# Kernel optimization log

Measured on AMD Instinct MI355X. Metric: run time of the kernel, lower is better.

The kernel has to match this reference:

```python
import jax, jax.numpy as jnp
import numpy as np

B, N, K = 4, 8192, 10
_DIMS = [(12, 64), (64, 64), (128, 64), (64, 64), (128, 64), (192, 1024), (1216, 256), (256, 256), (256, 128), (128, 2)]


def setup_inputs() -> dict:
    key = jax.random.key(0)
    keys = jax.random.split(key, 12)
    inp = {"targets": jax.random.normal(keys[0], (B, N, 3), dtype=jnp.float32)}
    for i, (ci, co) in enumerate(_DIMS):
        a = float(np.sqrt(0.75 / ci))  # init_params: uniform(-sqrt(0.75/fan_in), +)
        inp[f"w{i + 1}"] = jax.random.uniform(keys[i + 1], (ci, co), minval=-a, maxval=a, dtype=jnp.float32)
    inp["prelu_a"] = 0.25 * jnp.ones((10,), jnp.float32)  # nn.PReLU default slope
    return inp


def _prelu(x, a):
    return jnp.where(x >= 0, x, a * x)


def _graph_features(x, k):
    # x: [N, C] -> edge features [N, k, 2C] (knn gather, diff, concat center)
    x2 = jnp.sum(x * x, axis=-1)
    d = x2[:, None] + x2[None, :] - 2.0 * (x @ x.T)  # [N, N] sq dists
    _, idx = jax.lax.top_k(-d, k)  # k nearest (includes self)
    nb = x[idx]  # [N, k, C]
    xr = jnp.broadcast_to(x[:, None, :], nb.shape)
    return jnp.concatenate([nb - xr, xr], axis=-1)


def _edge_conv(x, wa_list, k):
    # x: [B, N, C]; shared-MLP on edge features then max over k neighbors
    f = jax.vmap(lambda xb: _graph_features(xb, k))(x)  # [B, N, k, 2C]
    for w, a in wa_list:
        f = _prelu(f @ w, a)
    return jnp.max(f, axis=-2)  # [B, N, Cout]


def _forward(targets, ws, pa):
    # loss_f(targets) = 0.5*||targets||^2  =>  targets_grad = targets
    g = jax.grad(lambda t: 0.5 * jnp.sum(t * t))(targets)
    x = jnp.concatenate([targets, g], axis=-1)  # [B, N, 6]; hidden_features=0
    x1 = _edge_conv(x, [(ws[0], pa[0]), (ws[1], pa[1])], K)
    x2 = _edge_conv(x1, [(ws[2], pa[2]), (ws[3], pa[3])], K)
    x3 = _edge_conv(x2, [(ws[4], pa[4])], K)
    x4 = jnp.concatenate([x1, x2, x3], axis=-1)  # [B, N, 192]
    x5 = _prelu(x4 @ ws[5], pa[5])  # [B, N, 1024]
    x5 = jnp.broadcast_to(jnp.max(x5, axis=-2, keepdims=True), x5.shape)  # global max, repeated
    y = jnp.concatenate([x1, x2, x3, x5], axis=-1)  # [B, N, 1216]
    for i in range(6, 10):  # dropout is identity at eval
        y = _prelu(y @ ws[i], pa[i])
    return y[..., : 2]  # lr = y[..., :num_losses*2]; hidden slice is empty


def reference(targets, w1, w2, w3, w4, w5, w6, w7, w8, w9, w10, prelu_a):
    ws = [w1, w2, w3, w4, w5, w6, w7, w8, w9, w10]
    return _forward(targets, ws, prelu_a)
```

## Files before the change

kernel.cpp:

```cpp
#include <hip/hip_runtime.h>
#include <math.h>

#define NPTS 8192
#define KNNK 10

typedef __attribute__((ext_vector_type(8))) short bf16x8s;
typedef __attribute__((ext_vector_type(4))) float f32x4;

__device__ __forceinline__ float preluf(float v, float a){ return v >= 0.f ? v : a*v; }
__device__ __forceinline__ float4 f4fma(float a, float4 b, float4 c){
  return make_float4(fmaf(a,b.x,c.x), fmaf(a,b.y,c.y), fmaf(a,b.z,c.z), fmaf(a,b.w,c.w));
}

__device__ __forceinline__ void gl_lds16(const void* g, void* l){
  __builtin_amdgcn_global_load_lds((const __attribute__((address_space(1))) void*)g,
                                   (__attribute__((address_space(3))) void*)l, 16, 0, 0);
}
__device__ __forceinline__ void gl_lds4(const void* g, void* l){
  __builtin_amdgcn_global_load_lds((const __attribute__((address_space(1))) void*)g,
                                   (__attribute__((address_space(3))) void*)l, 4, 0, 0);
}

__device__ __forceinline__ void kinsd2(double* bk, float& g9, float pbd9, float d, int j){
  if (__any(d < g9)) {
    double t = (double)d;
    t = __longlong_as_double(__double_as_longlong(t) | (unsigned long long)(unsigned)j);
    #pragma unroll
    for (int s=0;s<10;++s){
      double mn = fmin(bk[s], t);
      double mx = fmax(bk[s], t);
      bk[s] = mn; t = mx;
    }
    g9 = fminf((float)bk[9], pbd9);
  }
}

__device__ __forceinline__ unsigned bfsplit2(float a, float b, unsigned& lo2){
  unsigned ua = __float_as_uint(a), ub = __float_as_uint(b);
  unsigned ha = (ua + 0x7FFFu + ((ua>>16)&1u)) & 0xFFFF0000u;
  unsigned hb = (ub + 0x7FFFu + ((ub>>16)&1u)) & 0xFFFF0000u;
  float ra = a - __uint_as_float(ha);
  float rb = b - __uint_as_float(hb);
  unsigned la = __float_as_uint(ra), lb = __float_as_uint(rb);
  unsigned qa = (la + 0x7FFFu + ((la>>16)&1u)) >> 16;
  unsigned qb = (lb + 0x7FFFu + ((lb>>16)&1u)) & 0xFFFF0000u;
  lo2 = qa | qb;
  return (ha >> 16) | hb;
}

__global__ __launch_bounds__(256) void prep0_kernel(const float* __restrict__ T,
                                                    float* __restrict__ x0,
                                                    float* __restrict__ sqn){
  int p = blockIdx.x*256 + threadIdx.x;
  float t0 = T[p*3+0], t1 = T[p*3+1], t2 = T[p*3+2];
  *(float4*)(x0 + (size_t)p*4) = make_float4(t0,t1,t2,0.f);
  float s = fmaf(t0,t0,0.f); s = fmaf(t1,t1,s); s = fmaf(t2,t2,s); s = fmaf(0.f,0.f,s);
  sqn[p] = s;
}

__global__ __launch_bounds__(256, 4) void knn64_kernel(const unsigned short* __restrict__ Xh,
                                                       const unsigned short* __restrict__ Xl,
                                                       const float* __restrict__ sqn,
                                                       double* __restrict__ pk){
  __shared__ __align__(16) unsigned char smem[33792];
  float* sx2j = (float*)(smem + 32768);
  double* lst = (double*)smem;

  const int b   = blockIdx.y;
  const int q0  = blockIdx.x * 64;
  const int jh  = blockIdx.z;
  const int tid = threadIdx.x;
  const int L   = tid & 63;
  const int w   = tid >> 6;
  const int lm  = L & 15;
  const int kg  = L >> 4;

  const size_t bbase = (size_t)b * NPTS;
  const int qi = q0 + w*16 + lm;

  bf16x8s qh[2], ql[2];
  {
    const char* Qh = (const char*)Xh + (bbase + qi)*128;
    const char* Ql = (const char*)Xl + (bbase + qi)*128;
    #pragma unroll
    for (int kc=0;kc<2;++kc){
      qh[kc] = *(const bf16x8s*)(Qh + kc*64 + kg*16);
      ql[kc] = *(const bf16x8s*)(Ql + kc*64 + kg*16);
    }
  }
  const float x2q = sqn[bbase + qi];

  const int srow = L >> 3;
  const unsigned soff = (unsigned)(((L & 7) ^ srow) << 4);
  const char* srch = (const char*)Xh + (bbase + (size_t)jh*4096 + w*32 + srow)*128 + soff;
  const char* srcl = (const char*)Xl + (bbase + (size_t)jh*4096 + w*32 + srow)*128 + soff;
  const float* sx2jsrc = sqn + bbase + jh*4096 + w*64 + L;

  #pragma unroll
  for (int i=0;i<4;++i){
    gl_lds16(srch + i*1024, smem + w*4096 + i*1024);
    gl_lds16(srcl + i*1024, smem + 16384 + w*4096 + i*1024);
  }
  if (w < 2) gl_lds4(sx2jsrc, (char*)sx2j + w*256);

  double bk[10];
  float g9 = INFINITY, pbd9 = INFINITY;
  #pragma unroll
  for (int u=0;u<10;++u) bk[u] = (double)INFINITY;

  const char* xjh_c = (const char*)smem;
  const char* xjl_c = (const char*)smem + 16384;
  const unsigned swz = (unsigned)((lm & 7) << 4);

  for (int t = 0; t < 32; ++t) {
    __syncthreads();

    f32x4 acc[8];
    #pragma unroll
    for (int jb=0;jb<8;++jb) acc[jb] = (f32x4){0.f,0.f,0.f,0.f};

    #pragma unroll
    for (int kc=0;kc<2;++kc){
      const unsigned koff = (unsigned)(kc*64 + kg*16) ^ swz;
      #pragma unroll
      for (int jb=0;jb<8;++jb){
        const int rb = (jb*16 + lm)*128;
        bf16x8s jhf = *(const bf16x8s*)(xjh_c + rb + koff);
        bf16x8s jlf = *(const bf16x8s*)(xjl_c + rb + koff);
        acc[jb] = __builtin_amdgcn_mfma_f32_16x16x32_bf16(jhf, qh[kc], acc[jb], 0,0,0);
        acc[jb] = __builtin_amdgcn_mfma_f32_16x16x32_bf16(jlf, qh[kc], acc[jb], 0,0,0);
        acc[jb] = __builtin_amdgcn_mfma_f32_16x16x32_bf16(jhf, ql[kc], acc[jb], 0,0,0);
      }
    }
    __syncthreads();

    if (t < 31){
      const char* nh = srch + (size_t)(t+1)*16384;
      const char* nl = srcl + (size_t)(t+1)*16384;
      #pragma unroll
      for (int i=0;i<4;++i){
        gl_lds16(nh + i*1024, smem + w*4096 + i*1024);
        gl_lds16(nl + i*1024, smem + 16384 + w*4096 + i*1024);
      }
      if (w < 2) gl_lds4(sx2jsrc + (size_t)(t+1)*128, (char*)sx2j + ((t+1)&1)*512 + w*256);
    }

    const int j0 = jh*4096 + t*128;
    const float* x2jb = sx2j + (t&1)*128;

    #pragma unroll
    for (int jb=0;jb<8;++jb){
      float4 xj2 = *(const float4*)&x2jb[jb*16 + kg*4];
      f32x4 c = acc[jb];
      float4 dv = make_float4(x2q + xj2.x - 2.0f*c[0],
                              x2q + xj2.y - 2.0f*c[1],
                              x2q + xj2.z - 2.0f*c[2],
                              x2q + xj2.w - 2.0f*c[3]);
      float m4 = fminf(fminf(dv.x,dv.y), fminf(dv.z,dv.w));
      if (__any(m4 < g9)){
        const int jj = j0 + jb*16 + kg*4;
        kinsd2(bk, g9, pbd9, dv.x, jj);
        kinsd2(bk, g9, pbd9, dv.y, jj+1);
        kinsd2(bk, g9, pbd9, dv.z, jj+2);
        kinsd2(bk, g9, pbd9, dv.w, jj+3);
      }
      if (jb & 1){
        float d9 = (float)bk[9];
        float m  = fminf(d9, __shfl_xor(d9, 16));
        float mm = fminf(m,  __shfl_xor(m, 32));
        pbd9 = mm;
        g9 = mm;
      }
    }
  }

  __syncthreads();
  #pragma unroll
  for (int u=0;u<10;++u) lst[(size_t)(w*16 + lm)*40 + kg*10 + u] = bk[u];
  __syncthreads();
  if (tid < 64) {
    const double* row = &lst[(size_t)tid*40];
    int i0=0, i1=0, i2=0, i3=0;
    size_t base = ((size_t)jh*(4*NPTS) + bbase + q0 + tid)*10;
    #pragma unroll
    for (int u=0;u<10;++u){
      double ka = row[i0], kb2 = row[10+i1], kc2 = row[20+i2], kd2 = row[30+i3];
      bool tab = ka  < kb2; double mab = tab ? ka  : kb2;
      bool tcd = kc2 < kd2; double mcd = tcd ? kc2 : kd2;
      bool tt  = mab < mcd; double m   = tt  ? mab : mcd;
      pk[base+u] = m;
      i0 += (tt && tab)  ? 1 : 0;
      i1 += (tt && !tab) ? 1 : 0;
      i2 += (!tt && tcd) ? 1 : 0;
      i3 += (!tt && !tcd)? 1 : 0;
    }
  }
}

__global__ __launch_bounds__(256, 2) void knn4_kernel(const float* __restrict__ X,
                                                      const float* __restrict__ sqn,
                                                      double* __restrict__ pk){
  __shared__ __align__(16) float xqT[4*132];
  __shared__ __align__(16) float uni[10752];
  __shared__ float s_x2q[128];
  __shared__ float s_x2j[128];
  __shared__ float sbd[2][128];

  const int b   = blockIdx.y;
  const int q0  = blockIdx.x * 128;
  const int jh  = blockIdx.z;
  const int tid = threadIdx.x;
  const int tn  = tid & 15;
  const int tm  = tid >> 4;
  const int tq  = tid & 127;
  const int th  = tid >> 7;

  const float* Xb = X + (size_t)b * NPTS * 4;

  for (int i = tid; i < 128; i += 256) {
    float4 v = *(const float4*)(Xb + (size_t)(q0+i)*4);
    xqT[0*132+i] = v.x; xqT[1*132+i] = v.y; xqT[2*132+i] = v.z; xqT[3*132+i] = v.w;
  }
  if (tid < 128) s_x2q[tid] = sqn[b*NPTS + q0 + tid];

  const int sw  = ((tn>>2)&3) << 2;
  const int bp0 = (tn*8)     ^ sw;
  const int bp1 = (tn*8 + 4) ^ sw;

  double bk[10];
  float g9 = INFINITY, pbd9 = INFINITY;
  #pragma unroll
  for (int u=0;u<10;++u) bk[u] = (double)INFINITY;

  for (int t = 0; t < 32; ++t) {
    const int j0 = jh*4096 + t*128;
    for (int i = tid; i < 128; i += 256) {
      float4 v = *(const float4*)(Xb + (size_t)(j0+i)*4);
      int pj = i ^ (((i>>5)&3) << 2);
      uni[0*132+pj] = v.x; uni[1*132+pj] = v.y; uni[2*132+pj] = v.z; uni[3*132+pj] = v.w;
    }
    if (tid < 128) s_x2j[tid] = sqn[b*NPTS + j0 + tid];
    __syncthreads();

    float acc[8][8];
    #pragma unroll
    for (int i=0;i<8;++i)
      #pragma unroll
      for (int j=0;j<8;++j) acc[i][j] = 0.f;

    #pragma unroll
    for (int kk=0; kk<4; ++kk) {
      float av[8], bv[8];
      *(float4*)&av[0] = *(const float4*)&xqT[kk*132 + tm*8];
      *(float4*)&av[4] = *(const float4*)&xqT[kk*132 + tm*8 + 4];
      *(float4*)&bv[0] = *(const float4*)&uni[kk*132 + bp0];
      *(float4*)&bv[4] = *(const float4*)&uni[kk*132 + bp1];
      #pragma unroll
      for (int i=0;i<8;++i)
        #pragma unroll
        for (int j=0;j<8;++j)
          acc[i][j] = fmaf(av[i], bv[j], acc[i][j]);
    }
    __syncthreads();

    #pragma unroll
    for (int h=0; h<2; ++h) {
      if ((tn>>3) == h) {
        #pragma unroll
        for (int qi=0; qi<8; ++qi) {
          const int row = tm*8 + qi;
          const float xq2 = s_x2q[row];
          float vv[8];
          #pragma unroll
          for (int u=0;u<8;++u)
            vv[u] = xq2 + s_x2j[tn*8 + u] - 2.f*acc[qi][u];
          *(float4*)&uni[row*68 + (tn&7)*8]     = make_float4(vv[0],vv[1],vv[2],vv[3]);
          *(float4*)&uni[row*68 + (tn&7)*8 + 4] = make_float4(vv[4],vv[5],vv[6],vv[7]);
        }
      }
      __syncthreads();
      {
        const int jb0 = j0 + h*64 + th*32;
        #pragma unroll
        for (int c4=0;c4<8;++c4){
          float4 dv = *(const float4*)&uni[tq*68 + th*32 + c4*4];
          int jj = jb0 + c4*4;
          kinsd2(bk, g9, pbd9, dv.x, jj);
          kinsd2(bk, g9, pbd9, dv.y, jj+1);
          kinsd2(bk, g9, pbd9, dv.z, jj+2);
          kinsd2(bk, g9, pbd9, dv.w, jj+3);
        }
      }
      if (h == 1) sbd[th][tq] = (float)bk[9];
      __syncthreads();
      if (h == 1){
        pbd9 = sbd[1^th][tq];
        g9 = fminf((float)bk[9], pbd9);
      }
    }
  }

  double* lst = (double*)uni;
  #pragma unroll
  for (int u=0;u<10;++u) lst[tq*20 + th*10 + u] = bk[u];
  __syncthreads();
  if (tid < 128) {
    const double* row = &lst[tid*20];
    int ia=0, ib=0;
    size_t base = ((size_t)jh*(4*NPTS) + (size_t)b*NPTS + q0 + tid)*10;
    #pragma unroll
    for (int u=0;u<10;++u){
      double ka = row[ia], kb2 = row[10+ib];
      bool ta = ka < kb2;
      pk[base+u] = ta ? ka : kb2;
      ia += ta ? 1 : 0; ib += ta ? 0 : 1;
    }
  }
}

__global__ __launch_bounds__(256) void knnmerge_kernel(const double* __restrict__ pk,
                                                       int* __restrict__ idxout){
  int p = blockIdx.x*256 + threadIdx.x;
  const double* A = pk + (size_t)p*10;
  const double* B = pk + (size_t)(4*NPTS)*10 + (size_t)p*10;
  int ia=0, ib=0;
  int* op = idxout + (size_t)p*10;
  #pragma unroll
  for (int u=0;u<10;++u){
    double ka = A[ia], kb = B[ib];
    bool t = ka < kb;
    op[u] = (int)(__double_as_longlong(t ? ka : kb) & 8191LL);
    ia += t ? 1 : 0; ib += t ? 0 : 1;
  }
}

__global__ __launch_bounds__(256) void prepUD64_kernel(const float* __restrict__ XC, int cin,
                                                       const float* __restrict__ W,
                                                       float* __restrict__ U,
                                                       float* __restrict__ D){
  const int tid = threadIdx.x;
  const int w = tid >> 6, o = tid & 63;
  const int p = blockIdx.x*4 + w;
  const float* xr = XC + (size_t)p*192 + cin;
  float zu = 0.f, zd = 0.f;
  #pragma unroll
  for (int c=0;c<64;++c){
    float xc = xr[c];
    float wt = W[c*64 + o];
    float wb = W[(64+c)*64 + o];
    zu = fmaf(xc, wt, zu);
    zd = fmaf(xc, wb - wt, zd);
  }
  U[(size_t)p*64 + o] = zu;
  D[(size_t)p*64 + o] = zd;
}

__global__ __launch_bounds__(256) void prepUD12_kernel(const float* __restrict__ T,
                                                       const float* __restrict__ W1,
                                                       float* __restrict__ U,
                                                       float* __restrict__ D){
  int p = blockIdx.x*256 + threadIdx.x;
  float t[3] = {T[p*3+0], T[p*3+1], T[p*3+2]};
  const float4* W = (const float4*)W1;
  float4 u[16], q[16];
  #pragma unroll
  for (int o=0;o<16;++o){ u[o]=make_float4(0,0,0,0); q[o]=make_float4(0,0,0,0); }
  #pragma unroll
  for (int c=0;c<3;++c){
    const float tc = t[c];
    #pragma unroll
    for (int o=0;o<16;++o){
      float4 ws  = W[c*16+o],     ws2 = W[(c+3)*16+o];
      float4 wq  = W[(c+6)*16+o], wq2 = W[(c+9)*16+o];
      u[o] = f4fma(tc, make_float4(ws.x+ws2.x, ws.y+ws2.y, ws.z+ws2.z, ws.w+ws2.w), u[o]);
      q[o] = f4fma(tc, make_float4(wq.x+wq2.x, wq.y+wq2.y, wq.z+wq2.z, wq.w+wq2.w), q[o]);
    }
  }
  float4* up = (float4*)(U + (size_t)p*64);
  float4* dp = (float4*)(D + (size_t)p*64);
  #pragma unroll
  for (int o=0;o<16;++o){
    up[o] = u[o];
    dp[o] = make_float4(q[o].x-u[o].x, q[o].y-u[o].y, q[o].z-u[o].z, q[o].w-u[o].w);
  }
}

__global__ __launch_bounds__(256) void edge2w_kernel(const float* __restrict__ U,
                                                     const float* __restrict__ Dp,
                                                     const int* __restrict__ idx,
                                                     const float* __restrict__ Wb,
                                                     const float* __restrict__ PA, int paa, int pab,
                                                     float* __restrict__ out, int coff,
                                                     float* __restrict__ sqnout,
                                                     unsigned short* __restrict__ Xh,
                                                     unsigned short* __restrict__ Xl){
  __shared__ __align__(16) float sh[4][10][68];
  const int tid = threadIdx.x;
  const int w = tid >> 6, o = tid & 63;
  const int p = blockIdx.x*4 + w, b = p >> 13;
  const float aa = PA[paa], ab = PA[pab];

  float wreg[64];
  #pragma unroll
  for (int c=0;c<64;++c) wreg[c] = Wb[c*64 + o];

  const float dc = Dp[(size_t)p*64 + o];

  #pragma unroll
  for (int k=0;k<10;++k){
    int nb = idx[p*10 + k];
    float u = U[((size_t)(b<<13)+nb)*64 + o];
    sh[w][k][o] = preluf(u + dc, aa);
  }
  __syncthreads();

  float mx = -INFINITY;
  #pragma unroll 2
  for (int k=0;k<10;++k){
    float a0=0.f,a1=0.f,a2=0.f,a3=0.f;
    #pragma unroll
    for (int c4=0;c4<16;++c4){
      float4 hv = *(const float4*)&sh[w][k][c4*4];
      a0 = fmaf(hv.x, wreg[c4*4+0], a0);
      a1 = fmaf(hv.y, wreg[c4*4+1], a1);
      a2 = fmaf(hv.z, wreg[c4*4+2], a2);
      a3 = fmaf(hv.w, wreg[c4*4+3], a3);
    }
    float z = (a0+a1)+(a2+a3);
    mx = fmaxf(mx, preluf(z, ab));
  }
  out[(size_t)p*192 + coff + o] = mx;
  {
    unsigned um = __float_as_uint(mx);
    unsigned h  = (um + 0x7FFFu + ((um>>16)&1u)) & 0xFFFF0000u;
    float rr = mx - __uint_as_float(h);
    unsigned ur = __float_as_uint(rr);
    unsigned l  = (ur + 0x7FFFu + ((ur>>16)&1u)) >> 16;
    Xh[(size_t)p*64 + o] = (unsigned short)(h >> 16);
    Xl[(size_t)p*64 + o] = (unsigned short)l;
  }
  float sq = mx*mx;
  #pragma unroll
  for (int off=1; off<64; off<<=1) sq += __shfl_xor(sq, off);
  if (o == 0) sqnout[p] = sq;
}

__global__ __launch_bounds__(256) void edge1w_kernel(const float* __restrict__ U,
                                                     const float* __restrict__ Dp,
                                                     const int* __restrict__ idx,
                                                     const float* __restrict__ PA, int paa,
                                                     float* __restrict__ out, int coff){
  const int tid = threadIdx.x;
  const int w = tid >> 6, o = tid & 63;
  const int p = blockIdx.x*4 + w, b = p >> 13;
  const float aa = PA[paa];
  const float dc = Dp[(size_t)p*64 + o];
  float mx = -INFINITY;
  #pragma unroll
  for (int k=0;k<10;++k){
    int nb = idx[p*10 + k];
    float u = U[((size_t)(b<<13)+nb)*64 + o];
    mx = fmaxf(mx, preluf(u + dc, aa));
  }
  out[(size_t)p*192 + coff + o] = mx;
}

__global__ __launch_bounds__(256) void prepWall_kernel(const float* __restrict__ W6,
                                                       const float* __restrict__ W7,
                                                       const float* __restrict__ W8,
                                                       const float* __restrict__ W9,
                                                       unsigned short* __restrict__ Wh6, unsigned short* __restrict__ Wl6,
                                                       unsigned short* __restrict__ Wh7, unsigned short* __restrict__ Wl7,
                                                       unsigned short* __restrict__ Wh8, unsigned short* __restrict__ Wl8,
                                                       unsigned short* __restrict__ Wh9, unsigned short* __restrict__ Wl9){
  int bb = blockIdx.x;
  const float* W; unsigned short *Wh, *Wl; int K, N, k;
  if (bb < 192)      { W=W6; Wh=Wh6; Wl=Wl6; K=192; N=1024; k=bb; }
  else if (bb < 384) { W=W7; Wh=Wh7; Wl=Wl7; K=192; N=256;  k=bb-192; }
  else if (bb < 640) { W=W8; Wh=Wh8; Wl=Wl8; K=256; N=256;  k=bb-384; }
  else               { W=W9; Wh=Wh9; Wl=Wl9; K=256; N=128;  k=bb-640; }
  for (int n = threadIdx.x; n < N; n += 256){
    float v = W[(size_t)k*N + n];
    unsigned ua = __float_as_uint(v);
    unsigned h = (ua + 0x7FFFu + ((ua>>16)&1u)) & 0xFFFF0000u;
    float r = v - __uint_as_float(h);
    unsigned ub = __float_as_uint(r);
    unsigned l = (ub + 0x7FFFu + ((ub>>16)&1u)) >> 16;
    Wh[(size_t)n*K + k] = (unsigned short)(h >> 16);
    Wl[(size_t)n*K + k] = (unsigned short)l;
  }
}

template<int EPI>
__global__ __launch_bounds__(256, 2) void mgemm_kernel(const float* __restrict__ A, int lda,
                                                       const unsigned short* __restrict__ WhT,
                                                       const unsigned short* __restrict__ WlT,
                                                       int K,
                                                       float* __restrict__ C, int ldc,
                                                       const float* __restrict__ bias,
                                                       const float* __restrict__ PA, int pidx,
                                                       int Ntot){
  __shared__ __align__(16) unsigned char smem[73728];
  unsigned short* sa = (unsigned short*)smem;
  unsigned short* sb = (unsigned short*)(smem + 36864);
  float* cst = (float*)smem;

  const int tid = threadIdx.x;
  const int m0 = blockIdx.x*128, n0 = blockIdx.y*128;
  const int L = tid & 63, w = tid >> 6;
  const int lm = L & 15, kg = L >> 4;

  f32x4 acc[2][8];
  #pragma unroll
  for (int mt=0;mt<2;++mt)
    #pragma unroll
    for (int nt=0;nt<8;++nt) acc[mt][nt] = (f32x4){0.f,0.f,0.f,0.f};

  for (int c0 = 0; c0 < K; c0 += 64) {
    __syncthreads();
    #pragma unroll
    for (int s=0;s<8;++s){
      int e = tid + s*256;
      int r = e >> 4, kq = (e & 15) << 2;
      float4 v = *(const float4*)(A + (size_t)(m0+r)*lda + c0 + kq);
      unsigned lo01, lo23;
      unsigned hi01 = bfsplit2(v.x, v.y, lo01);
      unsigned hi23 = bfsplit2(v.z, v.w, lo23);
      uint2 hp; hp.x = hi01; hp.y = hi23;
      uint2 lp; lp.x = lo01; lp.y = lo23;
      *(uint2*)&sa[r*72 + kq]        = hp;
      *(uint2*)&sa[9216 + r*72 + kq] = lp;
    }
    #pragma unroll
    for (int s=0;s<4;++s){
      int e = tid + s*256;
      int col = e >> 3, ko = (e & 7) << 3;
      *(uint4*)&sb[col*72 + ko]        = *(const uint4*)&WhT[(size_t)(n0+col)*K + c0 + ko];
      *(uint4*)&sb[9216 + col*72 + ko] = *(const uint4*)&WlT[(size_t)(n0+col)*K + c0 + ko];
    }
    __syncthreads();

    #pragma unroll
    for (int kc=0;kc<2;++kc){
      const int ko = kc*32 + kg*8;
      bf16x8s ah[2], al[2];
      #pragma unroll
      for (int mt=0;mt<2;++mt){
        int q = w*32 + mt*16 + lm;
        ah[mt] = *(const bf16x8s*)&sa[q*72 + ko];
        al[mt] = *(const bf16x8s*)&sa[9216 + q*72 + ko];
      }
      #pragma unroll
      for (int nt=0;nt<8;++nt){
        int n = nt*16 + lm;
        bf16x8s bh = *(const bf16x8s*)&sb[n*72 + ko];
        bf16x8s bl = *(const bf16x8s*)&sb[9216 + n*72 + ko];
        #pragma unroll
        for (int mt=0;mt<2;++mt){
          acc[mt][nt] = __builtin_amdgcn_mfma_f32_16x16x32_bf16(ah[mt], bh, acc[mt][nt], 0,0,0);
          acc[mt][nt] = __builtin_amdgcn_mfma_f32_16x16x32_bf16(ah[mt], bl, acc[mt][nt], 0,0,0);
          acc[mt][nt] = __builtin_amdgcn_mfma_f32_16x16x32_bf16(al[mt], bh, acc[mt][nt], 0,0,0);
        }
      }
    }
  }
  __syncthreads();

  const float a = PA[pidx];
  if (EPI == 2) {
    #pragma unroll
    for (int nt=0;nt<8;++nt){
      f32x4 c0v = acc[0][nt], c1v = acc[1][nt];
      float m = -INFINITY;
      #pragma unroll
      for (int r=0;r<4;++r){ m = fmaxf(m, preluf(c0v[r], a)); m = fmaxf(m, preluf(c1v[r], a)); }
      m = fmaxf(m, __shfl_xor(m, 16));
      m = fmaxf(m, __shfl_xor(m, 32));
      if (kg == 0) cst[w*128 + nt*16 + lm] = m;
    }
    __syncthreads();
    if (tid < 128){
      float m = fmaxf(fmaxf(cst[tid], cst[128+tid]), fmaxf(cst[256+tid], cst[384+tid]));
      C[(size_t)blockIdx.x*Ntot + n0 + tid] = m;
    }
  } else {
    float bc[8];
    if (EPI == 1){
      int bb = m0 >> 13;
      #pragma unroll
      for (int nt=0;nt<8;++nt) bc[nt] = bias[bb*256 + n0 + nt*16 + lm];
    }
    #pragma unroll
    for (int mt=0;mt<2;++mt){
      #pragma unroll
      for (int nt=0;nt<8;++nt){
        f32x4 c = acc[mt][nt];
        int col = nt*16 + lm;
        #pragma unroll
        for (int r=0;r<4;++r){
          int row = w*32 + mt*16 + kg*4 + r;
          float v = c[r] + (EPI==1 ? bc[nt] : 0.f);
          cst[row*132 + col] = preluf(v, a);
        }
      }
    }
    __syncthreads();
    const int tm = tid & 15, tn = tid >> 4;
    #pragma unroll
    for (int i=0;i<8;++i){
      int row = tm*8 + i;
      float4 v0 = *(const float4*)&cst[row*132 + tn*8];
      float4 v1 = *(const float4*)&cst[row*132 + tn*8 + 4];
      float* cp = C + (size_t)(m0 + row)*ldc + n0 + tn*8;
      *(float4*)cp     = v0;
      *(float4*)(cp+4) = v1;
    }
  }
}

__global__ __launch_bounds__(256) void reduce_pmax(const float* __restrict__ pmax,
                                                   float* __restrict__ x5m){
  int t = blockIdx.x*256 + threadIdx.x;
  if (t < 4096) {
    int b = t >> 10, o = t & 1023;
    float m = -INFINITY;
    for (int mt=0; mt<64; ++mt) m = fmaxf(m, pmax[((size_t)(b*64+mt))*1024 + o]);
    x5m[t] = m;
  }
}

__global__ __launch_bounds__(256) void bias7_kernel(const float* __restrict__ x5m,
                                                    const float* __restrict__ W7,
                                                    float* __restrict__ b7){
  int b = blockIdx.x; int o = threadIdx.x;
  float s = 0.f;
  for (int j=0;j<1024;++j) s = fmaf(x5m[b*1024+j], W7[(size_t)(192+j)*256 + o], s);
  b7[b*256+o] = s;
}

__global__ __launch_bounds__(256) void final10_kernel(const float* __restrict__ y3,
                                                      const float* __restrict__ W10,
                                                      const float* __restrict__ PA,
                                                      float* __restrict__ out){
  int p = blockIdx.x*256 + threadIdx.x;
  const float4* r = (const float4*)(y3 + (size_t)p*128);
  float s0=0.f, s1=0.f;
  #pragma unroll
  for (int c4=0;c4<32;++c4){
    float4 v = r[c4];
    s0 = fmaf(v.x, W10[(c4*4+0)*2+0], s0); s1 = fmaf(v.x, W10[(c4*4+0)*2+1], s1);
    s0 = fmaf(v.y, W10[(c4*4+1)*2+0], s0); s1 = fmaf(v.y, W10[(c4*4+1)*2+1], s1);
    s0 = fmaf(v.z, W10[(c4*4+2)*2+0], s0); s1 = fmaf(v.z, W10[(c4*4+2)*2+1], s1);
    s0 = fmaf(v.w, W10[(c4*4+3)*2+0], s0); s1 = fmaf(v.w, W10[(c4*4+3)*2+1], s1);
  }
  float a = PA[9];
  out[p*2+0] = s0>=0.f? s0 : a*s0;
  out[p*2+1] = s1>=0.f? s1 : a*s1;
}

extern "C" void kernel_launch(void* const* d_in, const int* in_sizes, int n_in,
                              void* d_out, int out_size, void* d_ws, size_t ws_size,
                              hipStream_t stream) {
  const float* T   = (const float*)d_in[0];
  const float* W1  = (const float*)d_in[1];
  const float* W2  = (const float*)d_in[2];
  const float* W3  = (const float*)d_in[3];
  const float* W4  = (const float*)d_in[4];
  const float* W5  = (const float*)d_in[5];
  const float* W6  = (const float*)d_in[6];
  const float* W7  = (const float*)d_in[7];
  const float* W8  = (const float*)d_in[8];
  const float* W9  = (const float*)d_in[9];
  const float* W10 = (const float*)d_in[10];
  const float* PA  = (const float*)d_in[11];

  float* ws   = (float*)d_ws;
  float* x0   = ws + 0;
  float* sqn0 = ws + 131072;
  float* sqn1 = ws + 163840;
  float* sqn2 = ws + 196608;
  int*   idx0 = (int*)(ws + 229376);
  int*   idx1 = (int*)(ws + 557056);
  int*   idx2 = (int*)(ws + 884736);
  float* xcat = ws + 1212416;
  float* pmax = ws + 7503872;
  float* x5m  = ws + 7766016;
  float* b7   = ws + 7770112;
  float* y1   = ws + 7771136;
  float* y2   = ws + 16159744;
  float* y3   = xcat;
  float* U    = y1;
  float* D    = y2;
  double* pk  = (double*)y1;
  unsigned short* Xh = (unsigned short*)(y1 + 3145728);
  unsigned short* Xl = (unsigned short*)(y1 + 4194304);

  unsigned short* wsc = (unsigned short*)(ws + 229376);
  unsigned short* Wh6 = wsc;
  unsigned short* Wl6 = wsc + 196608;
  unsigned short* Wh7 = wsc + 393216;
  unsigned short* Wl7 = wsc + 442368;
  unsigned short* Wh8 = wsc + 491520;
  unsigned short* Wl8 = wsc + 557056;
  unsigned short* Wh9 = wsc + 622592;
  unsigned short* Wl9 = wsc + 655360;

  prep0_kernel<<<128, 256, 0, stream>>>(T, x0, sqn0);
  knn4_kernel<<<dim3(64,4,2), 256, 0, stream>>>(x0, sqn0, pk);
  knnmerge_kernel<<<128, 256, 0, stream>>>(pk, idx0);
  prepUD12_kernel<<<128, 256, 0, stream>>>(T, W1, U, D);
  edge2w_kernel<<<8192, 256, 0, stream>>>(U, D, idx0, W2, PA, 0, 1, xcat, 0, sqn1, Xh, Xl);

  knn64_kernel<<<dim3(128,4,2), 256, 0, stream>>>(Xh, Xl, sqn1, pk);
  knnmerge_kernel<<<128, 256, 0, stream>>>(pk, idx1);
  prepUD64_kernel<<<8192, 256, 0, stream>>>(xcat, 0, W3, U, D);
  edge2w_kernel<<<8192, 256, 0, stream>>>(U, D, idx1, W4, PA, 2, 3, xcat, 64, sqn2, Xh, Xl);

  knn64_kernel<<<dim3(128,4,2), 256, 0, stream>>>(Xh, Xl, sqn2, pk);
  knnmerge_kernel<<<128, 256, 0, stream>>>(pk, idx2);
  prepUD64_kernel<<<8192, 256, 0, stream>>>(xcat, 64, W5, U, D);
  edge1w_kernel<<<8192, 256, 0, stream>>>(U, D, idx2, PA, 4, xcat, 128);

  prepWall_kernel<<<896, 256, 0, stream>>>(W6, W7, W8, W9,
                                           Wh6, Wl6, Wh7, Wl7, Wh8, Wl8, Wh9, Wl9);

  mgemm_kernel<2><<<dim3(256,8), 256, 0, stream>>>(xcat, 192, Wh6, Wl6, 192, pmax, 0, nullptr, PA, 5, 1024);
  reduce_pmax<<<16, 256, 0, stream>>>(pmax, x5m);
  bias7_kernel<<<4, 256, 0, stream>>>(x5m, W7, b7);
  mgemm_kernel<1><<<dim3(256,2), 256, 0, stream>>>(xcat, 192, Wh7, Wl7, 192, y1, 256, b7, PA, 6, 0);
  mgemm_kernel<0><<<dim3(256,2), 256, 0, stream>>>(y1, 256, Wh8, Wl8, 256, y2, 256, nullptr, PA, 7, 0);
  mgemm_kernel<0><<<dim3(256,1), 256, 0, stream>>>(y2, 256, Wh9, Wl9, 256, y3, 128, nullptr, PA, 8, 0);
  final10_kernel<<<128, 256, 0, stream>>>(y3, W10, PA, (float*)d_out);
}
```

Before: 1.523 ms.

## Restructure first-layer kNN kernel: per-lane distances, async LDS double-buffering, 4-way candidate split

New measurement: 1.517 ms. About the same (-0.4%).

```diff
diff --git a/kernel.cpp b/kernel.cpp
--- a/kernel.cpp
+++ b/kernel.cpp
@@ -197,123 +197,113 @@
   }
 }
 
-__global__ __launch_bounds__(256, 2) void knn4_kernel(const float* __restrict__ X,
+__global__ __launch_bounds__(256, 4) void knn4_kernel(const float* __restrict__ X,
                                                       const float* __restrict__ sqn,
                                                       double* __restrict__ pk){
-  __shared__ __align__(16) float xqT[4*132];
-  __shared__ __align__(16) float uni[10752];
-  __shared__ float s_x2q[128];
-  __shared__ float s_x2j[128];
-  __shared__ float sbd[2][128];
+  __shared__ __align__(16) unsigned char smem[20480];
+  double* lst = (double*)smem;
 
   const int b   = blockIdx.y;
-  const int q0  = blockIdx.x * 128;
+  const int q0  = blockIdx.x * 64;
   const int jh  = blockIdx.z;
   const int tid = threadIdx.x;
-  const int tn  = tid & 15;
-  const int tm  = tid >> 4;
-  const int tq  = tid & 127;
-  const int th  = tid >> 7;
-
-  const float* Xb = X + (size_t)b * NPTS * 4;
-
-  for (int i = tid; i < 128; i += 256) {
-    float4 v = *(const float4*)(Xb + (size_t)(q0+i)*4);
-    xqT[0*132+i] = v.x; xqT[1*132+i] = v.y; xqT[2*132+i] = v.z; xqT[3*132+i] = v.w;
-  }
-  if (tid < 128) s_x2q[tid] = sqn[b*NPTS + q0 + tid];
-
-  const int sw  = ((tn>>2)&3) << 2;
-  const int bp0 = (tn*8)     ^ sw;
-  const int bp1 = (tn*8 + 4) ^ sw;
+  const int L   = tid & 63;
+  const int w   = tid >> 6;
+  const int lm  = L & 15;
+  const int kg  = L >> 4;
+
+  const size_t bbase = (size_t)b * NPTS;
+  const int qi = q0 + w*16 + lm;
+  const float4 q4 = *(const float4*)(X + (bbase + qi)*4);
+  const float x2q = sqn[bbase + qi];
+
+  const char* srcj  = (const char*)(X + (bbase + (size_t)jh*4096)*4);
+  const float* srcs = sqn + bbase + jh*4096;
+
+  gl_lds16(srcj + (size_t)(w*64 + L)*16, smem + w*1024);
+  gl_lds4 (srcs + w*64 + L, smem + 8192 + w*256);
 
   double bk[10];
   float g9 = INFINITY, pbd9 = INFINITY;
   #pragma unroll
   for (int u=0;u<10;++u) bk[u] = (double)INFINITY;
 
-  for (int t = 0; t < 32; ++t) {
-    const int j0 = jh*4096 + t*128;
-    for (int i = tid; i < 128; i += 256) {
-      float4 v = *(const float4*)(Xb + (size_t)(j0+i)*4);
-      int pj = i ^ (((i>>5)&3) << 2);
-      uni[0*132+pj] = v.x; uni[1*132+pj] = v.y; uni[2*132+pj] = v.z; uni[3*132+pj] = v.w;
-    }
-    if (tid < 128) s_x2j[tid] = sqn[b*NPTS + j0 + tid];
+  for (int t = 0; t < 16; ++t) {
     __syncthreads();
-
-    float acc[8][8];
-    #pragma unroll
-    for (int i=0;i<8;++i)
-      #pragma unroll
-      for (int j=0;j<8;++j) acc[i][j] = 0.f;
-
-    #pragma unroll
-    for (int kk=0; kk<4; ++kk) {
-      float av[8], bv[8];
-      *(float4*)&av[0] = *(const float4*)&xqT[kk*132 + tm*8];
-      *(float4*)&av[4] = *(const float4*)&xqT[kk*132 + tm*8 + 4];
-      *(float4*)&bv[0] = *(const float4*)&uni[kk*132 + bp0];
-      *(float4*)&bv[4] = *(const float4*)&uni[kk*132 + bp1];
-      #pragma unroll
-      for (int i=0;i<8;++i)
-        #pragma unroll
-        for (int j=0;j<8;++j)
-          acc[i][j] = fmaf(av[i], bv[j], acc[i][j]);
-    }
-    __syncthreads();
-
-    #pragma unroll
-    for (int h=0; h<2; ++h) {
-      if ((tn>>3) == h) {
-        #pragma unroll
-        for (int qi=0; qi<8; ++qi) {
-          const int row = tm*8 + qi;
-          const float xq2 = s_x2q[row];
-          float vv[8];
-          #pragma unroll
-          for (int u=0;u<8;++u)
-            vv[u] = xq2 + s_x2j[tn*8 + u] - 2.f*acc[qi][u];
-          *(float4*)&uni[row*68 + (tn&7)*8]     = make_float4(vv[0],vv[1],vv[2],vv[3]);
-          *(float4*)&uni[row*68 + (tn&7)*8 + 4] = make_float4(vv[4],vv[5],vv[6],vv[7]);
-        }
-      }
-      __syncthreads();
+    if (t < 15){
+      const int nb = (t+1)&1;
+      gl_lds16(srcj + (size_t)(t+1)*4096 + (size_t)(w*64 + L)*16, smem + nb*4096 + w*1024);
+      gl_lds4 (srcs + (t+1)*256 + w*64 + L, smem + 8192 + nb*1024 + w*256);
+    }
+    const float* xj  = (const float*)(smem + (t&1)*4096);
+    const float* x2j = (const float*)(smem + 8192 + (t&1)*1024);
+    const int j0 = jh*4096 + t*256;
+
+    #pragma unroll
+    for (int jb=0;jb<16;++jb){
+      const int r0 = jb*16 + kg*4;
+      float d0,d1,d2,d3;
       {
-        const int jb0 = j0 + h*64 + th*32;
-        #pragma unroll
-        for (int c4=0;c4<8;++c4){
-          float4 dv = *(const float4*)&uni[tq*68 + th*32 + c4*4];
-          int jj = jb0 + c4*4;
-          kinsd2(bk, g9, pbd9, dv.x, jj);
-          kinsd2(bk, g9, pbd9, dv.y, jj+1);
-          kinsd2(bk, g9, pbd9, dv.z, jj+2);
-          kinsd2(bk, g9, pbd9, dv.w, jj+3);
-        }
-      }
-      if (h == 1) sbd[th][tq] = (float)bk[9];
-      __syncthreads();
-      if (h == 1){
-        pbd9 = sbd[1^th][tq];
-        g9 = fminf((float)bk[9], pbd9);
-      }
-    }
-  }
-
-  double* lst = (double*)uni;
-  #pragma unroll
-  for (int u=0;u<10;++u) lst[tq*20 + th*10 + u] = bk[u];
+        float4 xv = *(const float4*)&xj[(r0+0)*4];
+        float acc = fmaf(q4.x, xv.x, 0.f); acc = fmaf(q4.y, xv.y, acc);
+        acc = fmaf(q4.z, xv.z, acc);       acc = fmaf(q4.w, xv.w, acc);
+        d0 = x2q + x2j[r0+0] - 2.f*acc;
+      }
+      {
+        float4 xv = *(const float4*)&xj[(r0+1)*4];
+        float acc = fmaf(q4.x, xv.x, 0.f); acc = fmaf(q4.y, xv.y, acc);
+        acc = fmaf(q4.z, xv.z, acc);       acc = fmaf(q4.w, xv.w, acc);
+        d1 = x2q + x2j[r0+1] - 2.f*acc;
+      }
+      {
+        float4 xv = *(const float4*)&xj[(r0+2)*4];
+        float acc = fmaf(q4.x, xv.x, 0.f); acc = fmaf(q4.y, xv.y, acc);
+        acc = fmaf(q4.z, xv.z, acc);       acc = fmaf(q4.w, xv.w, acc);
+        d2 = x2q + x2j[r0+2] - 2.f*acc;
+      }
+      {
+        float4 xv = *(const float4*)&xj[(r0+3)*4];
+        float acc = fmaf(q4.x, xv.x, 0.f); acc = fmaf(q4.y, xv.y, acc);
+        acc = fmaf(q4.z, xv.z, acc);       acc = fmaf(q4.w, xv.w, acc);
+        d3 = x2q + x2j[r0+3] - 2.f*acc;
+      }
+      float m4 = fminf(fminf(d0,d1), fminf(d2,d3));
+      if (__any(m4 < g9)){
+        const int jj = j0 + r0;
+        kinsd2(bk, g9, pbd9, d0, jj);
+        kinsd2(bk, g9, pbd9, d1, jj+1);
+        kinsd2(bk, g9, pbd9, d2, jj+2);
+        kinsd2(bk, g9, pbd9, d3, jj+3);
+      }
+      if (jb & 1){
+        float d9 = (float)bk[9];
+        float m  = fminf(d9, __shfl_xor(d9, 16));
+        float mm = fminf(m,  __shfl_xor(m, 32));
+        pbd9 = mm;
+        g9 = mm;
+      }
+    }
+  }
+
   __syncthreads();
-  if (tid < 128) {
-    const double* row = &lst[tid*20];
-    int ia=0, ib=0;
-    size_t base = ((size_t)jh*(4*NPTS) + (size_t)b*NPTS + q0 + tid)*10;
+  #pragma unroll
+  for (int u=0;u<10;++u) lst[(size_t)(w*16 + lm)*40 + kg*10 + u] = bk[u];
+  __syncthreads();
+  if (tid < 64) {
+    const double* row = &lst[(size_t)tid*40];
+    int i0=0, i1=0, i2=0, i3=0;
+    size_t base = ((size_t)jh*(4*NPTS) + bbase + q0 + tid)*10;
     #pragma unroll
     for (int u=0;u<10;++u){
-      double ka = row[ia], kb2 = row[10+ib];
-      bool ta = ka < kb2;
-      pk[base+u] = ta ? ka : kb2;
-      ia += ta ? 1 : 0; ib += ta ? 0 : 1;
+      double ka = row[i0], kb2 = row[10+i1], kc2 = row[20+i2], kd2 = row[30+i3];
+      bool tab = ka  < kb2; double mab = tab ? ka  : kb2;
+      bool tcd = kc2 < kd2; double mcd = tcd ? kc2 : kd2;
+      bool tt  = mab < mcd; double m   = tt  ? mab : mcd;
+      pk[base+u] = m;
+      i0 += (tt && tab)  ? 1 : 0;
+      i1 += (tt && !tab) ? 1 : 0;
+      i2 += (!tt && tcd) ? 1 : 0;
+      i3 += (!tt && !tcd)? 1 : 0;
     }
   }
 }
@@ -706,7 +696,7 @@
   unsigned short* Wl9 = wsc + 655360;
 
   prep0_kernel<<<128, 256, 0, stream>>>(T, x0, sqn0);
-  knn4_kernel<<<dim3(64,4,2), 256, 0, stream>>>(x0, sqn0, pk);
+  knn4_kernel<<<dim3(128,4,2), 256, 0, stream>>>(x0, sqn0, pk);
   knnmerge_kernel<<<128, 256, 0, stream>>>(pk, idx0);
   prepUD12_kernel<<<128, 256, 0, stream>>>(T, W1, U, D);
   edge2w_kernel<<<8192, 256, 0, stream>>>(U, D, idx0, W2, PA, 0, 1, xcat, 0, sqn1, Xh, Xl);
```
